# Kernel tuning notes

Hardware: AMD Instinct MI355X
Metric: run time of the kernel (lower is better)

## Reference

```python
import jax, jax.numpy as jnp
import numpy as np

B, N, D, C = 64, 512, 1024, 4  # batch, num_electrodes, d_model, num_classes
H = D // 2


def setup_inputs() -> dict:
    key = jax.random.key(0)
    ks = jax.random.split(key, 16)
    s = 0.02
    return {
        "Q": jax.random.normal(ks[0], (B, N, D), jnp.float32),
        "K": jax.random.normal(ks[1], (B, N, D), jnp.float32),
        "V": jax.random.normal(ks[2], (B, N, D), jnp.float32),
        "electrode_ids": jnp.arange(N, dtype=jnp.int64 if jax.config.jax_enable_x64 else jnp.int32),
        "emb": jax.random.normal(ks[3], (N, D), jnp.float32) * s,
        "dw1": jax.random.normal(ks[4], (H, D), jnp.float32) * s,
        "db1": jnp.zeros((H,), jnp.float32),
        "dw2": jax.random.normal(ks[5], (1, H), jnp.float32) * s,
        "db2": jnp.zeros((1,), jnp.float32),
        "sw1": jax.random.normal(ks[6], (H, D), jnp.float32) * s,
        "sb1": jnp.zeros((H,), jnp.float32),
        "sw2": jax.random.normal(ks[7], (1, H), jnp.float32) * s,
        "sb2": jnp.zeros((1,), jnp.float32),
        "dopamine_scale": jnp.asarray(1.0, jnp.float32),
        "serotonin_scale": jnp.asarray(1.0, jnp.float32),
        "fc_w": jax.random.normal(ks[8], (C, N * D), jnp.float32) * s,
        "fc_b": jnp.zeros((C,), jnp.float32),
    }


def reference(Q, K, V, electrode_ids, emb, dw1, db1, dw2, db2,
              sw1, sb1, sw2, sb2, dopamine_scale, serotonin_scale, fc_w, fc_b):
    e = emb[electrode_ids]                       # [N, D]
    Q = Q + e
    K = K + e
    V = V + e
    scale = jnp.sqrt(jnp.asarray(D, jnp.float32))
    scores = jnp.einsum('bnd,bmd->bnm', Q, K) / scale          # [B, N, N]
    probs = jax.nn.softmax(scores, axis=-1)
    entropy = -jnp.sum(probs * jnp.log(probs + 1e-6), axis=-1)  # [B, N]

    # dopamine MLP on Q tokens (eval mode -> dropout is identity)
    dh = jax.nn.relu(jnp.einsum('bnd,hd->bnh', Q, dw1) + db1)
    dopamine = jax.nn.sigmoid(jnp.einsum('bnh,oh->bno', dh, dw2) + db2)[..., 0]  # [B, N]

    # serotonin MLP on entropy broadcast to D identical features:
    # Linear(entropy * ones(D)) == entropy * W1.sum(axis=1) + b1 (same math, no [B,N,D] temp)
    sh = jax.nn.relu(entropy[..., None] * jnp.sum(sw1, axis=1) + sb1)            # [B, N, H]
    serotonin = jax.nn.sigmoid(jnp.einsum('bnh,oh->bno', sh, sw2) + sb2)[..., 0]  # [B, N]

    mod = dopamine_scale * dopamine[..., None] - serotonin_scale * serotonin[..., None]
    ms = scores + mod
    mu = jnp.mean(ms, axis=-1, keepdims=True)
    sd = jnp.std(ms, axis=-1, keepdims=True, ddof=1)  # torch.std default is unbiased
    ms = (ms - mu) / (sd + 1e-6)
    probs2 = jax.nn.softmax(ms, axis=-1)
    attn_out = jnp.einsum('bnm,bmd->bnd', probs2, V)   # [B, N, D]
    flat = attn_out.reshape(attn_out.shape[0], -1)      # [B, N*D]
    return flat @ fc_w.T + fc_b                          # [B, C]
```

## Files before the change

### kernel.cpp

```cpp
#include <hip/hip_runtime.h>

#define NN 512
#define ND 1024
#define NDW 524288
#define NBATCH 64

typedef __attribute__((ext_vector_type(8))) __bf16 bf16x8;
typedef __attribute__((ext_vector_type(4))) float f32x4;
typedef unsigned short u16;
typedef unsigned int u32;

__device__ __forceinline__ u16 f2bf(float x) {
    u32 u = __float_as_uint(x);
    u = (u + 0x7fffu + ((u >> 16) & 1u)) >> 16;
    return (u16)u;
}

union BF8 { bf16x8 v; u16 s[8]; };

__device__ __forceinline__ void dma16(const u16* g, const u16* l) {
    __builtin_amdgcn_global_load_lds(
        (const __attribute__((address_space(1))) u32*)(uintptr_t)g,
        (__attribute__((address_space(3))) u32*)(u32)(uintptr_t)l,
        16, 0, 0);
}

__global__ __launch_bounds__(256)
void prep_all(const float* __restrict__ K, const float* __restrict__ V,
              const int* __restrict__ eid, const float* __restrict__ emb,
              u16* __restrict__ Ke, u16* __restrict__ VT,
              float* __restrict__ out, const float* __restrict__ fcb)
{
    __shared__ u16 T[64 * 72];
    const int bb = blockIdx.x;
    const int tid = threadIdx.x;

    if (bb < 16384) {
        size_t f = ((size_t)bb * 256 + tid) * 8;
        int n = (int)((f >> 10) & (NN - 1));
        int col = (int)(f & (ND - 1));
        const float* ep = emb + (size_t)eid[n] * ND + col;
        float4 e0 = *(const float4*)ep, e1 = *(const float4*)(ep + 4);
        const float* kp = K + f;
        float4 x0 = *(const float4*)kp, x1 = *(const float4*)(kp + 4);
        union { uint4 u; u16 s[8]; } o;
        o.s[0]=f2bf(x0.x+e0.x); o.s[1]=f2bf(x0.y+e0.y); o.s[2]=f2bf(x0.z+e0.z); o.s[3]=f2bf(x0.w+e0.w);
        o.s[4]=f2bf(x1.x+e1.x); o.s[5]=f2bf(x1.y+e1.y); o.s[6]=f2bf(x1.z+e1.z); o.s[7]=f2bf(x1.w+e1.w);
        *(uint4*)(Ke + f) = o.u;
    } else if (bb < 16384 + 8192) {
        const int t = bb - 16384;
        const int n0 = (t & 7) * 64, d0 = ((t >> 3) & 15) * 64, b = t >> 7;
        {
            const int r = tid >> 2, cs = (tid & 3) * 16;
            const int n = n0 + r;
            const float* vp = V + ((size_t)b * NN + n) * ND + d0 + cs;
            const float* ep = emb + (size_t)eid[n] * ND + d0 + cs;
            #pragma unroll
            for (int j = 0; j < 4; ++j) {
                float4 v = *(const float4*)(vp + j * 4);
                float4 e = *(const float4*)(ep + j * 4);
                T[(cs + j*4 + 0) * 72 + r] = f2bf(v.x + e.x);
                T[(cs + j*4 + 1) * 72 + r] = f2bf(v.y + e.y);
                T[(cs + j*4 + 2) * 72 + r] = f2bf(v.z + e.z);
                T[(cs + j*4 + 3) * 72 + r] = f2bf(v.w + e.w);
            }
        }
        __syncthreads();
        {
            const int dr = tid >> 2, ms = (tid & 3) * 16;
            u16* dst = VT + ((size_t)b * ND + d0 + dr) * NN + n0 + ms;
            *(uint4*)dst       = *(const uint4*)&T[dr * 72 + ms];
            *(uint4*)(dst + 8) = *(const uint4*)&T[dr * 72 + ms + 8];
        }
    } else {
        if (tid < NBATCH * 4) out[tid] = fcb[tid & 3];
    }
}

__global__ __launch_bounds__(256)
void nma_attn(const float* __restrict__ Q, const int* __restrict__ eid,
              const float* __restrict__ emb, const u16* __restrict__ Ke,
              const u16* __restrict__ VT, const float* __restrict__ fcw,
              float* __restrict__ out)
{
    __shared__ __align__(16) u16 KV[NN * 32];
    __shared__ __align__(16) u16 Ps[32 * 520];
    __shared__ float red[4][32][4];
    __shared__ float rowM[32], rowInv[32], rowRden[32];

    const int tid  = threadIdx.x;
    const int w    = tid >> 6;
    const int lane = tid & 63;
    const int q    = lane >> 4;
    const int l15  = lane & 15;
    const int rr   = lane >> 2;
    const int seg  = lane & 3;
    const int bid  = blockIdx.x;
    const int jj   = bid >> 3;
    const int b    = (bid & 7) + ((jj >> 4) << 3);
    const int i0   = (jj & 15) * 32;
    const size_t bOff = (size_t)b * NN * ND;
    const int wrow = w * 128;

    const float* Qr0 = Q + bOff + (size_t)(i0 + l15) * ND;
    const float* Qr1 = Q + bOff + (size_t)(i0 + 16 + l15) * ND;
    const float* Er0 = emb + (size_t)eid[i0 + l15] * ND;
    const float* Er1 = emb + (size_t)eid[i0 + 16 + l15] * ND;

    const u16* KeB = Ke + bOff;
    const u16* VTB = VT + (size_t)b * ND * NN;

#define DMA_KE(KC) do {                                                         \
    _Pragma("unroll")                                                           \
    for (int ii_ = 0; ii_ < 8; ++ii_)                                           \
        dma16(KeB + (size_t)(wrow + ii_ * 16 + rr) * ND + (KC) * 32 + seg * 8,  \
              &KV[(wrow + ii_ * 16) * 32]);                                     \
    } while (0)

#define DMA_VT(H, MC) do {                                                      \
    _Pragma("unroll")                                                           \
    for (int ii_ = 0; ii_ < 8; ++ii_)                                           \
        dma16(VTB + (size_t)((H) * 512 + wrow + ii_ * 16 + rr) * NN             \
                  + (MC) * 32 + seg * 8,                                        \
              &KV[(wrow + ii_ * 16) * 32]);                                     \
    } while (0)

#define LOADQ(DST, KOFF) do {                                                   \
    DST[0] = *(const float4*)(Qr0 + (KOFF));                                    \
    DST[1] = *(const float4*)(Qr0 + (KOFF) + 4);                                \
    DST[2] = *(const float4*)(Er0 + (KOFF));                                    \
    DST[3] = *(const float4*)(Er0 + (KOFF) + 4);                                \
    DST[4] = *(const float4*)(Qr1 + (KOFF));                                    \
    DST[5] = *(const float4*)(Qr1 + (KOFF) + 4);                                \
    DST[6] = *(const float4*)(Er1 + (KOFF));                                    \
    DST[7] = *(const float4*)(Er1 + (KOFF) + 4);                                \
    } while (0)

    f32x4 acc[2][8];
    #pragma unroll
    for (int it = 0; it < 2; ++it)
        #pragma unroll
        for (int mt = 0; mt < 8; ++mt)
            acc[it][mt] = (f32x4){0.f, 0.f, 0.f, 0.f};

    float4 cur[8], nxt[8];
    {
        LOADQ(cur, q * 8);
        DMA_KE(0);
    }

#define P2BODY(KC, CUR, NXT) do {                                               \
    asm volatile("s_waitcnt vmcnt(0)" ::: "memory");    \
    bf16x8 bfr[8];                                                              \
    _Pragma("unroll")                                                           \
    for (int mt = 0; mt < 8; ++mt)                                              \
        bfr[mt] = *(const bf16x8*)&KV[(wrow + mt * 16 + l15) * 32 + q * 8];     \
    BF8 a0u, a1u;                                                               \
    a0u.s[0]=f2bf(CUR[0].x+CUR[2].x); a0u.s[1]=f2bf(CUR[0].y+CUR[2].y);         \
    a0u.s[2]=f2bf(CUR[0].z+CUR[2].z); a0u.s[3]=f2bf(CUR[0].w+CUR[2].w);         \
    a0u.s[4]=f2bf(CUR[1].x+CUR[3].x); a0u.s[5]=f2bf(CUR[1].y+CUR[3].y);         \
    a0u.s[6]=f2bf(CUR[1].z+CUR[3].z); a0u.s[7]=f2bf(CUR[1].w+CUR[3].w);         \
    a1u.s[0]=f2bf(CUR[4].x+CUR[6].x); a1u.s[1]=f2bf(CUR[4].y+CUR[6].y);         \
    a1u.s[2]=f2bf(CUR[4].z+CUR[6].z); a1u.s[3]=f2bf(CUR[4].w+CUR[6].w);         \
    a1u.s[4]=f2bf(CUR[5].x+CUR[7].x); a1u.s[5]=f2bf(CUR[5].y+CUR[7].y);         \
    a1u.s[6]=f2bf(CUR[5].z+CUR[7].z); a1u.s[7]=f2bf(CUR[5].w+CUR[7].w);         \
    asm volatile("s_waitcnt lgkmcnt(0)" ::: "memory");    \
    if ((KC) < 31) {                                                            \
        DMA_KE((KC) + 1);                    \
        LOADQ(NXT, ((KC) + 1) * 32 + q * 8);       \
    }                                                                           \
    _Pragma("unroll")                                                           \
    for (int mt = 0; mt < 8; ++mt) {                                            \
        acc[0][mt] = __builtin_amdgcn_mfma_f32_16x16x32_bf16(a0u.v, bfr[mt], acc[0][mt], 0, 0, 0); \
        acc[1][mt] = __builtin_amdgcn_mfma_f32_16x16x32_bf16(a1u.v, bfr[mt], acc[1][mt], 0, 0, 0); \
    } } while (0)

    for (int kc = 0; kc < 32; kc += 2) {
        P2BODY(kc, cur, nxt);
        P2BODY(kc + 1, nxt, cur);
    }

    const float SC = 0.03125f;
    #pragma unroll
    for (int it = 0; it < 2; ++it)
        #pragma unroll
        for (int mt = 0; mt < 8; ++mt) {
            acc[it][mt][0] *= SC; acc[it][mt][1] *= SC;
            acc[it][mt][2] *= SC; acc[it][mt][3] *= SC;
        }
    float ssum[2][4], ssq[2][4], smax[2][4];
    #pragma unroll
    for (int it = 0; it < 2; ++it)
        #pragma unroll
        for (int r = 0; r < 4; ++r) {
            float s = 0.f, s2 = 0.f, mx = -3.4e38f;
            #pragma unroll
            for (int mt = 0; mt < 8; ++mt) {
                float v = acc[it][mt][r];
                s += v; s2 += v * v; mx = fmaxf(mx, v);
            }
            #pragma unroll
            for (int d = 1; d < 16; d <<= 1) {
                s  += __shfl_xor(s, d);
                s2 += __shfl_xor(s2, d);
                mx  = fmaxf(mx, __shfl_xor(mx, d));
            }
            ssum[it][r] = s; ssq[it][r] = s2; smax[it][r] = mx;
        }
    if (l15 == 0) {
        #pragma unroll
        for (int it = 0; it < 2; ++it)
            #pragma unroll
            for (int r = 0; r < 4; ++r) {
                int i = it * 16 + q * 4 + r;
                red[w][i][0] = ssum[it][r];
                red[w][i][1] = ssq[it][r];
                red[w][i][2] = smax[it][r];
            }
    }
    __syncthreads();
    if (tid < 32) {
        float s  = red[0][tid][0] + red[1][tid][0] + red[2][tid][0] + red[3][tid][0];
        float s2 = red[0][tid][1] + red[1][tid][1] + red[2][tid][1] + red[3][tid][1];
        float mx = fmaxf(fmaxf(red[0][tid][2], red[1][tid][2]),
                         fmaxf(red[2][tid][2], red[3][tid][2]));
        float mu  = s * (1.f / 512.f);
        float var = fmaxf((s2 - s * mu) * (1.f / 511.f), 0.f);
        float sd  = sqrtf(var);
        rowM[tid]   = mx;
        rowInv[tid] = 1.f / (sd + 1e-6f);
    }
    __syncthreads();
    float dsum[2][4];
    #pragma unroll
    for (int it = 0; it < 2; ++it)
        #pragma unroll
        for (int r = 0; r < 4; ++r) {
            int i = it * 16 + q * 4 + r;
            float M = rowM[i], inv = rowInv[i];
            float s = 0.f;
            #pragma unroll
            for (int mt = 0; mt < 8; ++mt) {
                float e = __expf((acc[it][mt][r] - M) * inv);
                acc[it][mt][r] = e; s += e;
            }
            #pragma unroll
            for (int d = 1; d < 16; d <<= 1) s += __shfl_xor(s, d);
            dsum[it][r] = s;
        }
    if (l15 == 0) {
        #pragma unroll
        for (int it = 0; it < 2; ++it)
            #pragma unroll
            for (int r = 0; r < 4; ++r)
                red[w][it * 16 + q * 4 + r][0] = dsum[it][r];
    }
    __syncthreads();
    if (tid < 32)
        rowRden[tid] = 1.f / (red[0][tid][0] + red[1][tid][0] + red[2][tid][0] + red[3][tid][0]);
    __syncthreads();
    #pragma unroll
    for (int it = 0; it < 2; ++it)
        #pragma unroll
        for (int r = 0; r < 4; ++r) {
            int i = it * 16 + q * 4 + r;
            float rd = rowRden[i];
            #pragma unroll
            for (int mt = 0; mt < 8; ++mt) {
                int m = w * 128 + mt * 16 + l15;
                Ps[i * 520 + m] = f2bf(acc[it][mt][r] * rd);
            }
        }
    __syncthreads();

    DMA_VT(0, 0);
    float fsum[4] = {0.f, 0.f, 0.f, 0.f};
    for (int h = 0; h < 2; ++h) {
        f32x4 oacc[2][8];
        #pragma unroll
        for (int it = 0; it < 2; ++it)
            #pragma unroll
            for (int dt = 0; dt < 8; ++dt)
                oacc[it][dt] = (f32x4){0.f, 0.f, 0.f, 0.f};
        for (int mc = 0; mc < 16; ++mc) {
            bf16x8 p0 = *(const bf16x8*)&Ps[l15 * 520 + mc * 32 + q * 8];
            bf16x8 p1 = *(const bf16x8*)&Ps[(16 + l15) * 520 + mc * 32 + q * 8];
            asm volatile("s_waitcnt vmcnt(0)" ::: "memory");
            bf16x8 bfr[8];
            #pragma unroll
            for (int dt = 0; dt < 8; ++dt)
                bfr[dt] = *(const bf16x8*)&KV[(wrow + dt * 16 + l15) * 32 + q * 8];
            asm volatile("s_waitcnt lgkmcnt(0)" ::: "memory");
            const int j = h * 16 + mc;
            if (j < 31) {
                const int jn = j + 1;
                DMA_VT(jn >> 4, jn & 15);
            }
            #pragma unroll
            for (int dt = 0; dt < 8; ++dt) {
                oacc[0][dt] = __builtin_amdgcn_mfma_f32_16x16x32_bf16(p0, bfr[dt], oacc[0][dt], 0, 0, 0);
                oacc[1][dt] = __builtin_amdgcn_mfma_f32_16x16x32_bf16(p1, bfr[dt], oacc[1][dt], 0, 0, 0);
            }
        }
        #pragma unroll
        for (int it = 0; it < 2; ++it) {
            #pragma unroll
            for (int r = 0; r < 4; ++r) {
                const int iglob = i0 + it * 16 + q * 4 + r;
                const float* fr = fcw + (size_t)iglob * ND + (h * 512 + wrow + l15);
                #pragma unroll
                for (int dt = 0; dt < 8; ++dt) {
                    const float o = oacc[it][dt][r];
                    fsum[0] += o * fr[dt * 16];
                    fsum[1] += o * fr[(size_t)NDW + dt * 16];
                    fsum[2] += o * fr[(size_t)2 * NDW + dt * 16];
                    fsum[3] += o * fr[(size_t)3 * NDW + dt * 16];
                }
            }
        }
    }
    #pragma unroll
    for (int c = 0; c < 4; ++c)
        #pragma unroll
        for (int d = 1; d < 64; d <<= 1)
            fsum[c] += __shfl_xor(fsum[c], d);
    if (lane == 0) {
        red[w][0][0] = fsum[0]; red[w][0][1] = fsum[1];
        red[w][0][2] = fsum[2]; red[w][0][3] = fsum[3];
    }
    __syncthreads();
    if (tid < 4) {
        float s = red[0][0][tid] + red[1][0][tid] + red[2][0][tid] + red[3][0][tid];
        atomicAdd(&out[b * 4 + tid], s);
    }
#undef P2BODY
#undef LOADQ
#undef DMA_KE
#undef DMA_VT
}

extern "C" void kernel_launch(void* const* d_in, const int* in_sizes, int n_in,
                              void* d_out, int out_size, void* d_ws, size_t ws_size,
                              hipStream_t stream) {
    (void)in_sizes; (void)n_in; (void)ws_size; (void)out_size;
    const float* Q   = (const float*)d_in[0];
    const float* K   = (const float*)d_in[1];
    const float* V   = (const float*)d_in[2];
    const int*   eid = (const int*)d_in[3];
    const float* emb = (const float*)d_in[4];
    const float* fcw = (const float*)d_in[15];
    const float* fcb = (const float*)d_in[16];
    float* out = (float*)d_out;

    u16* Ke = (u16*)d_ws;
    u16* VT = Ke + (size_t)NBATCH * NN * ND;

    prep_all<<<dim3(16384 + 8192 + 1), dim3(256), 0, stream>>>(
        K, V, eid, emb, Ke, VT, out, fcb);
    nma_attn<<<dim3(1024), dim3(256), 0, stream>>>(Q, eid, emb, Ke, VT, fcw, out);
}
```

Before: 717.2 us.

## Precompute bf16 Q+emb in prep kernel and vectorize V transpose LDS writes

The prep kernel now also writes Q plus the electrode embedding as bf16 into a workspace buffer. The attention kernel then loads bf16x8 A-fragments directly instead of loading fp32 Q and emb and converting them inside the MFMA loop. This removes per-iteration conversion ALU work and halves the Q bytes read in the attention kernel, at the cost of an extra 64MB write and 64MB read pass in prep. The V transpose also packs two bf16 values per 32-bit LDS store, where it previously used scalar 16-bit scattered stores.

```diff
diff --git a/kernel.cpp b/kernel.cpp
--- a/kernel.cpp
+++ b/kernel.cpp
@@ -15,8 +15,6 @@
     u = (u + 0x7fffu + ((u >> 16) & 1u)) >> 16;
     return (u16)u;
 }
-
-union BF8 { bf16x8 v; u16 s[8]; };
 
 __device__ __forceinline__ void dma16(const u16* g, const u16* l) {
     __builtin_amdgcn_global_load_lds(
@@ -26,9 +24,10 @@
 }
 
 __global__ __launch_bounds__(256)
-void prep_all(const float* __restrict__ K, const float* __restrict__ V,
-              const int* __restrict__ eid, const float* __restrict__ emb,
-              u16* __restrict__ Ke, u16* __restrict__ VT,
+void prep_all(const float* __restrict__ Q, const float* __restrict__ K,
+              const float* __restrict__ V, const int* __restrict__ eid,
+              const float* __restrict__ emb,
+              u16* __restrict__ Qe, u16* __restrict__ Ke, u16* __restrict__ VT,
               float* __restrict__ out, const float* __restrict__ fcb)
 {
     __shared__ u16 T[64 * 72];
@@ -41,28 +40,45 @@
         int col = (int)(f & (ND - 1));
         const float* ep = emb + (size_t)eid[n] * ND + col;
         float4 e0 = *(const float4*)ep, e1 = *(const float4*)(ep + 4);
-        const float* kp = K + f;
-        float4 x0 = *(const float4*)kp, x1 = *(const float4*)(kp + 4);
-        union { uint4 u; u16 s[8]; } o;
-        o.s[0]=f2bf(x0.x+e0.x); o.s[1]=f2bf(x0.y+e0.y); o.s[2]=f2bf(x0.z+e0.z); o.s[3]=f2bf(x0.w+e0.w);
-        o.s[4]=f2bf(x1.x+e1.x); o.s[5]=f2bf(x1.y+e1.y); o.s[6]=f2bf(x1.z+e1.z); o.s[7]=f2bf(x1.w+e1.w);
-        *(uint4*)(Ke + f) = o.u;
+        {
+            const float* qp = Q + f;
+            float4 x0 = *(const float4*)qp, x1 = *(const float4*)(qp + 4);
+            union { uint4 u; u16 s[8]; } o;
+            o.s[0]=f2bf(x0.x+e0.x); o.s[1]=f2bf(x0.y+e0.y); o.s[2]=f2bf(x0.z+e0.z); o.s[3]=f2bf(x0.w+e0.w);
+            o.s[4]=f2bf(x1.x+e1.x); o.s[5]=f2bf(x1.y+e1.y); o.s[6]=f2bf(x1.z+e1.z); o.s[7]=f2bf(x1.w+e1.w);
+            *(uint4*)(Qe + f) = o.u;
+        }
+        {
+            const float* kp = K + f;
+            float4 x0 = *(const float4*)kp, x1 = *(const float4*)(kp + 4);
+            union { uint4 u; u16 s[8]; } o;
+            o.s[0]=f2bf(x0.x+e0.x); o.s[1]=f2bf(x0.y+e0.y); o.s[2]=f2bf(x0.z+e0.z); o.s[3]=f2bf(x0.w+e0.w);
+            o.s[4]=f2bf(x1.x+e1.x); o.s[5]=f2bf(x1.y+e1.y); o.s[6]=f2bf(x1.z+e1.z); o.s[7]=f2bf(x1.w+e1.w);
+            *(uint4*)(Ke + f) = o.u;
+        }
     } else if (bb < 16384 + 8192) {
         const int t = bb - 16384;
         const int n0 = (t & 7) * 64, d0 = ((t >> 3) & 15) * 64, b = t >> 7;
         {
-            const int r = tid >> 2, cs = (tid & 3) * 16;
-            const int n = n0 + r;
-            const float* vp = V + ((size_t)b * NN + n) * ND + d0 + cs;
-            const float* ep = emb + (size_t)eid[n] * ND + d0 + cs;
-            #pragma unroll
-            for (int j = 0; j < 4; ++j) {
-                float4 v = *(const float4*)(vp + j * 4);
-                float4 e = *(const float4*)(ep + j * 4);
-                T[(cs + j*4 + 0) * 72 + r] = f2bf(v.x + e.x);
-                T[(cs + j*4 + 1) * 72 + r] = f2bf(v.y + e.y);
-                T[(cs + j*4 + 2) * 72 + r] = f2bf(v.z + e.z);
-                T[(cs + j*4 + 3) * 72 + r] = f2bf(v.w + e.w);
+            const int r2 = (tid & 31) * 2;
+            const int cg = tid >> 5;
+            const int na = n0 + r2, nb = n0 + r2 + 1;
+            const float* vp0 = V + ((size_t)b * NN + na) * ND + d0 + cg * 8;
+            const float* vp1 = V + ((size_t)b * NN + nb) * ND + d0 + cg * 8;
+            const float* ep0 = emb + (size_t)eid[na] * ND + d0 + cg * 8;
+            const float* ep1 = emb + (size_t)eid[nb] * ND + d0 + cg * 8;
+            float4 a0 = *(const float4*)vp0,       a1 = *(const float4*)(vp0 + 4);
+            float4 b0 = *(const float4*)vp1,       b1 = *(const float4*)(vp1 + 4);
+            float4 x0 = *(const float4*)ep0,       x1 = *(const float4*)(ep0 + 4);
+            float4 y0 = *(const float4*)ep1,       y1 = *(const float4*)(ep1 + 4);
+            float lo[8] = {a0.x+x0.x, a0.y+x0.y, a0.z+x0.z, a0.w+x0.w,
+                           a1.x+x1.x, a1.y+x1.y, a1.z+x1.z, a1.w+x1.w};
+            float hi[8] = {b0.x+y0.x, b0.y+y0.y, b0.z+y0.z, b0.w+y0.w,
+                           b1.x+y1.x, b1.y+y1.y, b1.z+y1.z, b1.w+y1.w};
+            #pragma unroll
+            for (int j = 0; j < 8; ++j) {
+                u32 pk = (u32)f2bf(lo[j]) | ((u32)f2bf(hi[j]) << 16);
+                *(u32*)&T[(cg * 8 + j) * 72 + r2] = pk;
             }
         }
         __syncthreads();
@@ -78,8 +94,7 @@
 }
 
 __global__ __launch_bounds__(256)
-void nma_attn(const float* __restrict__ Q, const int* __restrict__ eid,
-              const float* __restrict__ emb, const u16* __restrict__ Ke,
+void nma_attn(const u16* __restrict__ Qe, const u16* __restrict__ Ke,
               const u16* __restrict__ VT, const float* __restrict__ fcw,
               float* __restrict__ out)
 {
@@ -102,11 +117,8 @@
     const size_t bOff = (size_t)b * NN * ND;
     const int wrow = w * 128;
 
-    const float* Qr0 = Q + bOff + (size_t)(i0 + l15) * ND;
-    const float* Qr1 = Q + bOff + (size_t)(i0 + 16 + l15) * ND;
-    const float* Er0 = emb + (size_t)eid[i0 + l15] * ND;
-    const float* Er1 = emb + (size_t)eid[i0 + 16 + l15] * ND;
-
+    const u16* aP0 = Qe + bOff + (size_t)(i0 + l15) * ND + q * 8;
+    const u16* aP1 = aP0 + (size_t)16 * ND;
     const u16* KeB = Ke + bOff;
     const u16* VTB = VT + (size_t)b * ND * NN;
 
@@ -125,17 +137,6 @@
               &KV[(wrow + ii_ * 16) * 32]);                                     \
     } while (0)
 
-#define LOADQ(DST, KOFF) do {                                                   \
-    DST[0] = *(const float4*)(Qr0 + (KOFF));                                    \
-    DST[1] = *(const float4*)(Qr0 + (KOFF) + 4);                                \
-    DST[2] = *(const float4*)(Er0 + (KOFF));                                    \
-    DST[3] = *(const float4*)(Er0 + (KOFF) + 4);                                \
-    DST[4] = *(const float4*)(Qr1 + (KOFF));                                    \
-    DST[5] = *(const float4*)(Qr1 + (KOFF) + 4);                                \
-    DST[6] = *(const float4*)(Er1 + (KOFF));                                    \
-    DST[7] = *(const float4*)(Er1 + (KOFF) + 4);                                \
-    } while (0)
-
     f32x4 acc[2][8];
     #pragma unroll
     for (int it = 0; it < 2; ++it)
@@ -143,41 +144,34 @@
         for (int mt = 0; mt < 8; ++mt)
             acc[it][mt] = (f32x4){0.f, 0.f, 0.f, 0.f};
 
-    float4 cur[8], nxt[8];
+    bf16x8 qc0, qc1, qn0, qn1;
     {
-        LOADQ(cur, q * 8);
+        qc0 = *(const bf16x8*)aP0;
+        qc1 = *(const bf16x8*)aP1;
         DMA_KE(0);
     }
 
-#define P2BODY(KC, CUR, NXT) do {                                               \
-    asm volatile("s_waitcnt vmcnt(0)" ::: "memory");    \
+#define P2BODY(KC, C0, C1, N0, N1) do {                                         \
+    asm volatile("s_waitcnt vmcnt(0)" ::: "memory");   \
     bf16x8 bfr[8];                                                              \
     _Pragma("unroll")                                                           \
     for (int mt = 0; mt < 8; ++mt)                                              \
         bfr[mt] = *(const bf16x8*)&KV[(wrow + mt * 16 + l15) * 32 + q * 8];     \
-    BF8 a0u, a1u;                                                               \
-    a0u.s[0]=f2bf(CUR[0].x+CUR[2].x); a0u.s[1]=f2bf(CUR[0].y+CUR[2].y);         \
-    a0u.s[2]=f2bf(CUR[0].z+CUR[2].z); a0u.s[3]=f2bf(CUR[0].w+CUR[2].w);         \
-    a0u.s[4]=f2bf(CUR[1].x+CUR[3].x); a0u.s[5]=f2bf(CUR[1].y+CUR[3].y);         \
-    a0u.s[6]=f2bf(CUR[1].z+CUR[3].z); a0u.s[7]=f2bf(CUR[1].w+CUR[3].w);         \
-    a1u.s[0]=f2bf(CUR[4].x+CUR[6].x); a1u.s[1]=f2bf(CUR[4].y+CUR[6].y);         \
-    a1u.s[2]=f2bf(CUR[4].z+CUR[6].z); a1u.s[3]=f2bf(CUR[4].w+CUR[6].w);         \
-    a1u.s[4]=f2bf(CUR[5].x+CUR[7].x); a1u.s[5]=f2bf(CUR[5].y+CUR[7].y);         \
-    a1u.s[6]=f2bf(CUR[5].z+CUR[7].z); a1u.s[7]=f2bf(CUR[5].w+CUR[7].w);         \
     asm volatile("s_waitcnt lgkmcnt(0)" ::: "memory");    \
     if ((KC) < 31) {                                                            \
         DMA_KE((KC) + 1);                    \
-        LOADQ(NXT, ((KC) + 1) * 32 + q * 8);       \
+        N0 = *(const bf16x8*)(aP0 + ((KC) + 1) * 32);    \
+        N1 = *(const bf16x8*)(aP1 + ((KC) + 1) * 32);                           \
     }                                                                           \
     _Pragma("unroll")                                                           \
     for (int mt = 0; mt < 8; ++mt) {                                            \
-        acc[0][mt] = __builtin_amdgcn_mfma_f32_16x16x32_bf16(a0u.v, bfr[mt], acc[0][mt], 0, 0, 0); \
-        acc[1][mt] = __builtin_amdgcn_mfma_f32_16x16x32_bf16(a1u.v, bfr[mt], acc[1][mt], 0, 0, 0); \
+        acc[0][mt] = __builtin_amdgcn_mfma_f32_16x16x32_bf16(C0, bfr[mt], acc[0][mt], 0, 0, 0); \
+        acc[1][mt] = __builtin_amdgcn_mfma_f32_16x16x32_bf16(C1, bfr[mt], acc[1][mt], 0, 0, 0); \
     } } while (0)
 
     for (int kc = 0; kc < 32; kc += 2) {
-        P2BODY(kc, cur, nxt);
-        P2BODY(kc + 1, nxt, cur);
+        P2BODY(kc,     qc0, qc1, qn0, qn1);
+        P2BODY(kc + 1, qn0, qn1, qc0, qc1);
     }
 
     const float SC = 0.03125f;
@@ -334,7 +328,6 @@
         atomicAdd(&out[b * 4 + tid], s);
     }
 #undef P2BODY
-#undef LOADQ
 #undef DMA_KE
 #undef DMA_VT
 }
@@ -352,10 +345,11 @@
     const float* fcb = (const float*)d_in[16];
     float* out = (float*)d_out;
 
-    u16* Ke = (u16*)d_ws;
+    u16* Qe = (u16*)d_ws;
+    u16* Ke = Qe + (size_t)NBATCH * NN * ND;
     u16* VT = Ke + (size_t)NBATCH * NN * ND;
 
     prep_all<<<dim3(16384 + 8192 + 1), dim3(256), 0, stream>>>(
-        K, V, eid, emb, Ke, VT, out, fcb);
-    nma_attn<<<dim3(1024), dim3(256), 0, stream>>>(Q, eid, emb, Ke, VT, fcw, out);
-}
+        Q, K, V, eid, emb, Qe, Ke, VT, out, fcb);
+    nma_attn<<<dim3(1024), dim3(256), 0, stream>>>(Qe, Ke, VT, fcw, out);
+}
```

Measured after the change: 681.4 us. 5.0% less time.
